# Kernel optimization log

Hardware: AMD Instinct MI355X
Metric: run time of the kernel (lower is better)

## Reference

```python
import jax, jax.numpy as jnp
import numpy as np

B, S, D, H = 2, 2048, 1024, 16
DH = D // H

def setup_inputs() -> dict:
    key = jax.random.key(0)
    ks = jax.random.split(key, 6)
    scale = 0.02
    return {
        "x":  jax.random.normal(ks[0], (B, S, D), jnp.float32),
        "Wq": jax.random.normal(ks[1], (D, D), jnp.float32) * scale,
        "Wk": jax.random.normal(ks[2], (D, D), jnp.float32) * scale,
        "Wv": jax.random.normal(ks[3], (D, D), jnp.float32) * scale,
        "Wo": jax.random.normal(ks[4], (D, D), jnp.float32) * scale,
        "bo": jnp.zeros((D,), jnp.float32),
    }

def reference(x, Wq, Wk, Wv, Wo, bo):
    b, s, d = x.shape
    h, dh = H, DH
    # projections -> [b, h, s, dh]
    def split_heads(t):
        return t.reshape(b, s, h, dh).transpose(0, 2, 1, 3)
    q = split_heads(x @ Wq)
    k = split_heads(x @ Wk)
    v = split_heads(x @ Wv)
    # scaled causal attention
    scores = jnp.einsum('bhqd,bhkd->bhqk', q, k) / jnp.sqrt(jnp.float32(dh))
    causal = jnp.tril(jnp.ones((s, s), bool))
    scores = jnp.where(causal[None, None], scores, -jnp.inf)
    attn = jax.nn.softmax(scores, axis=-1)
    # dropout p=0.0 -> identity
    ctx = jnp.einsum('bhqk,bhkd->bhqd', attn, v)
    ctx = ctx.transpose(0, 2, 1, 3).reshape(b, s, d)
    return ctx @ Wo + bo
```

## Files before the change

### kernel.cpp

```cpp
#include <hip/hip_runtime.h>


typedef _Float16 f16;
typedef _Float16 f16x8 __attribute__((ext_vector_type(8)));
typedef _Float16 f16x4 __attribute__((ext_vector_type(4)));
typedef float    f32x4 __attribute__((ext_vector_type(4)));

__device__ __forceinline__ void gload16(const void* g, void* l) {
  __builtin_amdgcn_global_load_lds(
      (const __attribute__((address_space(1))) void*)g,
      (__attribute__((address_space(3))) void*)l, 16, 0, 0);
}

__global__ void cvt_x(const float* __restrict__ x, f16* __restrict__ xb) {
  int idx = blockIdx.x * 256 + threadIdx.x;
  float4 v = ((const float4*)x)[idx];
  f16x4 o = { (f16)v.x, (f16)v.y, (f16)v.z, (f16)v.w };
  ((f16x4*)xb)[idx] = o;
}

__global__ void cvt_w(const float* __restrict__ W0, const float* __restrict__ W1,
                      const float* __restrict__ W2, const float* __restrict__ W3,
                      f16* __restrict__ T0, f16* __restrict__ T1,
                      f16* __restrict__ T2, f16* __restrict__ T3) {
  const float* W = blockIdx.z == 0 ? W0 : blockIdx.z == 1 ? W1 : blockIdx.z == 2 ? W2 : W3;
  f16*        Tt = blockIdx.z == 0 ? T0 : blockIdx.z == 1 ? T1 : blockIdx.z == 2 ? T2 : T3;
  __shared__ f16 tile[64][65];
  int tid = threadIdx.x;
  int k0 = blockIdx.y * 64, n0 = blockIdx.x * 64;
  int rr = tid >> 4, cc = (tid & 15) * 4;
#pragma unroll
  for (int p = 0; p < 4; ++p) {
    int r = rr + p * 16;
    float4 v = *(const float4*)(W + (size_t)(k0 + r) * 1024 + n0 + cc);
    tile[r][cc + 0] = (f16)v.x; tile[r][cc + 1] = (f16)v.y;
    tile[r][cc + 2] = (f16)v.z; tile[r][cc + 3] = (f16)v.w;
  }
  __syncthreads();
#pragma unroll
  for (int p = 0; p < 4; ++p) {
    int r = rr + p * 16;
    f16x4 v;
#pragma unroll
    for (int j = 0; j < 4; ++j) v[j] = tile[cc + j][r];
    *(f16x4*)(Tt + (size_t)(n0 + r) * 1024 + k0 + cc) = v;
  }
}

template <int MODE>
__global__ __launch_bounds__(256, 2)
void gemm_k(const f16* __restrict__ A, const f16* __restrict__ Bt,
            f16* __restrict__ oQ, f16* __restrict__ oK, f16* __restrict__ oV,
            float* __restrict__ oO, const float* __restrict__ bias) {
  constexpr int Kd = 1024;
  constexpr int BN = (MODE == 2) ? 64 : 128;
  constexpr int NF = BN / 32;
  __shared__ f16 smem[128 * 64 + BN * 64];
  f16* sA = smem;
  f16* sB = smem + 128 * 64;
  const int tid = threadIdx.x;
  const int lane = tid & 63, wid = tid >> 6;
  const int wr = wid >> 1, wc = wid & 1;
  const int bm = blockIdx.y * 128, bn = blockIdx.x * BN;

  f32x4 acc[4][NF] = {};

  for (int k0 = 0; k0 < Kd; k0 += 64) {
#pragma unroll
    for (int p = 0; p < 4; ++p) {
      int c = p * 256 + tid;
      int row = c >> 3;
      int gc = (c & 7) ^ (row & 7);
      gload16(A + (size_t)(bm + row) * Kd + k0 + gc * 8, sA + c * 8);
    }
#pragma unroll
    for (int p = 0; p < NF; ++p) {
      int c = p * 256 + tid;
      int row = c >> 3;
      int gc = (c & 7) ^ (row & 7);
      gload16(Bt + (size_t)(bn + row) * Kd + k0 + gc * 8, sB + c * 8);
    }
    __syncthreads();
#pragma unroll
    for (int ks = 0; ks < 2; ++ks) {
      f16x8 af[4], bf[NF];
#pragma unroll
      for (int m = 0; m < 4; ++m) {
        int row = wr * 64 + m * 16 + (lane & 15);
        int j = (ks * 4 + (lane >> 4)) ^ (row & 7);
        af[m] = *(const f16x8*)((const char*)sA + row * 128 + j * 16);
      }
#pragma unroll
      for (int n = 0; n < NF; ++n) {
        int row = wc * (BN / 2) + n * 16 + (lane & 15);
        int j = (ks * 4 + (lane >> 4)) ^ (row & 7);
        bf[n] = *(const f16x8*)((const char*)sB + row * 128 + j * 16);
      }
#pragma unroll
      for (int m = 0; m < 4; ++m)
#pragma unroll
        for (int n = 0; n < NF; ++n)
          acc[m][n] = __builtin_amdgcn_mfma_f32_16x16x32_f16(af[m], bf[n], acc[m][n], 0, 0, 0);
    }
    __syncthreads();
  }

  if constexpr (MODE == 2) {
#pragma unroll
    for (int m = 0; m < 4; ++m) {
      int rbase = bm + wr * 64 + m * 16 + ((lane >> 4) << 2);
#pragma unroll
      for (int n = 0; n < NF; ++n) {
        int ncol = bn + wc * (BN / 2) + n * 16 + (lane & 15);
        float bv = bias[ncol];
#pragma unroll
        for (int i = 0; i < 4; ++i)
          oO[(size_t)(rbase + i) * 1024 + ncol] = acc[m][n][i] + bv;
      }
    }
  } else {
    const int seg = bn >> 10;
    if (seg < 2) {
      f16* dst = seg == 0 ? oQ : oK;
#pragma unroll
      for (int m = 0; m < 4; ++m) {
        int rbase = bm + wr * 64 + m * 16 + ((lane >> 4) << 2);
#pragma unroll
        for (int n = 0; n < NF; ++n) {
          int ncol = (bn & 1023) + wc * 64 + n * 16 + (lane & 15);
          int h = ncol >> 6, dh = ncol & 63;
#pragma unroll
          for (int i = 0; i < 4; ++i) {
            int rr = rbase + i;
            int b = rr >> 11, s = rr & 2047;
            dst[(((size_t)(b * 16 + h) * 2048 + s) << 6) + dh] = (f16)acc[m][n][i];
          }
        }
      }
    } else {
      f16* T64 = smem;
      int b = bm >> 11, sbase = bm & 2047;
      int bnl = bn & 1023;
#pragma unroll
      for (int p = 0; p < 2; ++p) {
        if (wr == p) {
#pragma unroll
          for (int m = 0; m < 4; ++m)
#pragma unroll
            for (int n = 0; n < NF; ++n)
#pragma unroll
              for (int i = 0; i < 4; ++i) {
                int rl = m * 16 + ((lane >> 4) << 2) + i;
                int col = wc * 64 + n * 16 + (lane & 15);
                T64[rl * 132 + col] = (f16)acc[m][n][i];
              }
        }
        __syncthreads();
#pragma unroll
        for (int it = 0; it < 4; ++it) {
          int oc = it * 256 + tid;
          int ocol = oc >> 3;
          int och = oc & 7;
          f16x8 v;
#pragma unroll
          for (int j = 0; j < 8; ++j) v[j] = T64[(och * 8 + j) * 132 + ocol];
          int ncol = bnl + ocol;
          int h = ncol >> 6, dh = ncol & 63;
          *(f16x8*)(oV + ((size_t)((b * 16 + h) * 64 + dh) << 11) + sbase + p * 64 + och * 8) = v;
        }
        __syncthreads();
      }
    }
  }
}

__global__ __launch_bounds__(256, 2)
void attn_k(const f16* __restrict__ Q, const f16* __restrict__ Kg,
            const f16* __restrict__ Vt, f16* __restrict__ ctx) {
  __shared__ f16 sK[64 * 64];
  __shared__ f16 sV[64 * 64];
  __shared__ f16 sP[4][16 * 64];
  const int tid = threadIdx.x, lane = tid & 63, wid = tid >> 6;
  const int bh = blockIdx.y;
  const int b = bh >> 4, h = bh & 15;
  const int qt = ((bh >> 3) & 1) ? (31 - (int)blockIdx.x) : (int)blockIdx.x;
  const f16* Qb = Q + ((size_t)bh << 17);
  const f16* Kb = Kg + ((size_t)bh << 17);
  const f16* Vb = Vt + ((size_t)bh << 17);
  const float SC = 0.1803368801f;

  const int qbase = qt * 64 + wid * 16;
  const int qg = qbase + (lane & 15);
  const int qmax_w = qbase + 15;

  const int qrow_a = qbase + (lane & 15);
  f16x8 qf[2];
  qf[0] = *(const f16x8*)(Qb + (size_t)qrow_a * 64 + ((lane >> 4) << 3));
  qf[1] = *(const f16x8*)(Qb + (size_t)qrow_a * 64 + 32 + ((lane >> 4) << 3));

  f32x4 acc[4] = {};
  float m_run = -INFINITY, l_run = 0.f;

  for (int kt = 0; kt <= qt; ++kt) {
#pragma unroll
    for (int p = 0; p < 2; ++p) {
      int c = p * 256 + tid;
      int row = c >> 3;
      int gc = (c & 7) ^ (row & 7);
      gload16(Kb + (size_t)(kt * 64 + row) * 64 + gc * 8, sK + c * 8);
      gload16(Vb + (size_t)row * 2048 + kt * 64 + gc * 8, sV + c * 8);
    }
    __syncthreads();

    f32x4 sf[4];
#pragma unroll
    for (int kc = 0; kc < 4; ++kc) {
      if (kt * 64 + kc * 16 <= qmax_w) {
        f32x4 z = {};
#pragma unroll
        for (int ks = 0; ks < 2; ++ks) {
          int row = kc * 16 + (lane & 15);
          int j = (ks * 4 + (lane >> 4)) ^ (row & 7);
          f16x8 kf = *(const f16x8*)((const char*)sK + row * 128 + j * 16);
          z = __builtin_amdgcn_mfma_f32_16x16x32_f16(kf, qf[ks], z, 0, 0, 0);
        }
        sf[kc] = z;
      } else {
        sf[kc] = (f32x4){-1e30f, -1e30f, -1e30f, -1e30f};
      }
    }
#pragma unroll
    for (int kc = 0; kc < 4; ++kc) {
      if (kt * 64 + kc * 16 + 15 > qbase) {
#pragma unroll
        for (int i = 0; i < 4; ++i) {
          int kg = kt * 64 + kc * 16 + ((lane >> 4) << 2) + i;
          sf[kc][i] = (kg <= qg) ? sf[kc][i] * SC : -1e30f;
        }
      } else {
#pragma unroll
        for (int i = 0; i < 4; ++i) sf[kc][i] *= SC;
      }
    }
    float v01 = fmaxf(fmaxf(sf[0][0], sf[0][1]), fmaxf(sf[0][2], sf[0][3]));
    float v23 = fmaxf(fmaxf(sf[1][0], sf[1][1]), fmaxf(sf[1][2], sf[1][3]));
    float v45 = fmaxf(fmaxf(sf[2][0], sf[2][1]), fmaxf(sf[2][2], sf[2][3]));
    float v67 = fmaxf(fmaxf(sf[3][0], sf[3][1]), fmaxf(sf[3][2], sf[3][3]));
    float v = fmaxf(fmaxf(v01, v23), fmaxf(v45, v67));
    v = fmaxf(v, __shfl_xor(v, 16));
    v = fmaxf(v, __shfl_xor(v, 32));
    float mn = fmaxf(m_run, v);
    float scl = __builtin_amdgcn_exp2f(m_run - mn);
    m_run = mn;
    float ls = 0.f;
#pragma unroll
    for (int kc = 0; kc < 4; ++kc)
#pragma unroll
      for (int i = 0; i < 4; ++i) {
        float p = __builtin_amdgcn_exp2f(sf[kc][i] - mn);
        sf[kc][i] = p;
        ls += p;
      }
    ls += __shfl_xor(ls, 16);
    ls += __shfl_xor(ls, 32);
    l_run = l_run * scl + ls;
#pragma unroll
    for (int i = 0; i < 4; ++i) {
      float sb = __shfl(scl, ((lane >> 4) << 2) + i);
#pragma unroll
      for (int d = 0; d < 4; ++d) acc[d][i] *= sb;
    }
    char* Pw = (char*)(sP[wid]);
#pragma unroll
    for (int kc = 0; kc < 4; ++kc) {
      int kbase = kc * 16 + ((lane >> 4) << 2);
      int ch = kbase >> 3;
      f16x4 pv = { (f16)sf[kc][0], (f16)sf[kc][1], (f16)sf[kc][2], (f16)sf[kc][3] };
      *(f16x4*)(Pw + (lane & 15) * 128 + ((ch ^ (lane & 7)) << 4) + ((kbase & 7) << 1)) = pv;
    }
#pragma unroll
    for (int kk = 0; kk < 2; ++kk) {
      if (kt * 64 + kk * 32 <= qmax_w) {
        int prow = lane & 15;
        int pj = (kk * 4 + (lane >> 4)) ^ (prow & 7);
        f16x8 pa = *(const f16x8*)(Pw + prow * 128 + pj * 16);
#pragma unroll
        for (int d = 0; d < 4; ++d) {
          int vrow = d * 16 + (lane & 15);
          int vj = (kk * 4 + (lane >> 4)) ^ (vrow & 7);
          f16x8 vf = *(const f16x8*)((const char*)sV + vrow * 128 + vj * 16);
          acc[d] = __builtin_amdgcn_mfma_f32_16x16x32_f16(pa, vf, acc[d], 0, 0, 0);
        }
      }
    }
    __syncthreads();
  }
#pragma unroll
  for (int i = 0; i < 4; ++i) {
    float lb = __shfl(l_run, ((lane >> 4) << 2) + i);
    float r = 1.f / lb;
    int s = qbase + ((lane >> 4) << 2) + i;
#pragma unroll
    for (int d = 0; d < 4; ++d) {
      float val = acc[d][i] * r;
      ctx[((size_t)(b * 2048 + s) << 10) + (h << 6) + (d << 4) + (lane & 15)] = (f16)val;
    }
  }
}

extern "C" void kernel_launch(void* const* d_in, const int* in_sizes, int n_in,
                              void* d_out, int out_size, void* d_ws, size_t ws_size,
                              hipStream_t stream) {
  const float* x  = (const float*)d_in[0];
  const float* Wq = (const float*)d_in[1];
  const float* Wk = (const float*)d_in[2];
  const float* Wv = (const float*)d_in[3];
  const float* Wo = (const float*)d_in[4];
  const float* bo = (const float*)d_in[5];
  char* ws = (char*)d_ws;
  f16* xb   = (f16*)(ws);
  f16* Wcat = (f16*)(ws + ((size_t)8  << 20));
  f16* Wot  = (f16*)(ws + ((size_t)14 << 20));
  f16* Qb   = (f16*)(ws + ((size_t)16 << 20));
  f16* Kb   = (f16*)(ws + ((size_t)24 << 20));
  f16* Vtb  = (f16*)(ws + ((size_t)32 << 20));
  f16* ctx  = (f16*)(ws + ((size_t)40 << 20));
  const size_t MM = (size_t)1024 * 1024;

  hipLaunchKernelGGL(cvt_x, dim3(4096), dim3(256), 0, stream, x, xb);
  hipLaunchKernelGGL(cvt_w, dim3(16, 16, 4), dim3(256), 0, stream,
                     Wq, Wk, Wv, Wo, Wcat, Wcat + MM, Wcat + 2 * MM, Wot);
  hipLaunchKernelGGL((gemm_k<0>), dim3(24, 32), dim3(256), 0, stream,
                     xb, Wcat, Qb, Kb, Vtb, nullptr, nullptr);
  hipLaunchKernelGGL(attn_k, dim3(32, 32), dim3(256), 0, stream, Qb, Kb, Vtb, ctx);
  hipLaunchKernelGGL((gemm_k<2>), dim3(16, 32), dim3(256), 0, stream,
                     ctx, Wot, nullptr, nullptr, nullptr, (float*)d_out, bo);
}
```

Baseline: 188.2 us.

## Double attention query tile to 128 rows so each K/V load serves two row groups

Each attention block now handles 128 query rows instead of 64, with every wave owning two 16-row groups that keep separate softmax state and accumulators. Each K/V tile staged in shared memory is reused by twice as many queries, roughly halving the global-to-LDS K/V traffic and the barrier count per unit of work. The costs are half as many blocks (512), more registers per thread under a two-blocks-per-CU launch bound, and the two groups of a wave running one after the other within each K tile.

```diff
diff --git a/kernel.cpp b/kernel.cpp
--- a/kernel.cpp
+++ b/kernel.cpp
@@ -183,25 +183,28 @@
   const int tid = threadIdx.x, lane = tid & 63, wid = tid >> 6;
   const int bh = blockIdx.y;
   const int b = bh >> 4, h = bh & 15;
-  const int qt = ((bh >> 3) & 1) ? (31 - (int)blockIdx.x) : (int)blockIdx.x;
+  const int qt = ((bh >> 4) & 1) ? (15 - (int)blockIdx.x) : (int)blockIdx.x;
   const f16* Qb = Q + ((size_t)bh << 17);
   const f16* Kb = Kg + ((size_t)bh << 17);
   const f16* Vb = Vt + ((size_t)bh << 17);
   const float SC = 0.1803368801f;
 
-  const int qbase = qt * 64 + wid * 16;
-  const int qg = qbase + (lane & 15);
-  const int qmax_w = qbase + 15;
-
-  const int qrow_a = qbase + (lane & 15);
-  f16x8 qf[2];
-  qf[0] = *(const f16x8*)(Qb + (size_t)qrow_a * 64 + ((lane >> 4) << 3));
-  qf[1] = *(const f16x8*)(Qb + (size_t)qrow_a * 64 + 32 + ((lane >> 4) << 3));
-
-  f32x4 acc[4] = {};
-  float m_run = -INFINITY, l_run = 0.f;
-
-  for (int kt = 0; kt <= qt; ++kt) {
+  int qbase[2];
+  qbase[0] = qt * 128 + wid * 32;
+  qbase[1] = qbase[0] + 16;
+  f16x8 qf[2][2];
+#pragma unroll
+  for (int g = 0; g < 2; ++g) {
+    const f16* qp = Qb + (size_t)(qbase[g] + (lane & 15)) * 64 + ((lane >> 4) << 3);
+    qf[g][0] = *(const f16x8*)(qp);
+    qf[g][1] = *(const f16x8*)(qp + 32);
+  }
+
+  f32x4 acc[2][4] = {};
+  float m_run[2] = {-INFINITY, -INFINITY}, l_run[2] = {0.f, 0.f};
+  const int nkt = 2 * qt + 2;
+
+  for (int kt = 0; kt < nkt; ++kt) {
 #pragma unroll
     for (int p = 0; p < 2; ++p) {
       int c = p * 256 + tid;
@@ -212,100 +215,110 @@
     }
     __syncthreads();
 
-    f32x4 sf[4];
-#pragma unroll
-    for (int kc = 0; kc < 4; ++kc) {
-      if (kt * 64 + kc * 16 <= qmax_w) {
-        f32x4 z = {};
-#pragma unroll
-        for (int ks = 0; ks < 2; ++ks) {
-          int row = kc * 16 + (lane & 15);
-          int j = (ks * 4 + (lane >> 4)) ^ (row & 7);
-          f16x8 kf = *(const f16x8*)((const char*)sK + row * 128 + j * 16);
-          z = __builtin_amdgcn_mfma_f32_16x16x32_f16(kf, qf[ks], z, 0, 0, 0);
-        }
-        sf[kc] = z;
-      } else {
-        sf[kc] = (f32x4){-1e30f, -1e30f, -1e30f, -1e30f};
-      }
-    }
-#pragma unroll
-    for (int kc = 0; kc < 4; ++kc) {
-      if (kt * 64 + kc * 16 + 15 > qbase) {
+    char* Pw = (char*)(sP[wid]);
+#pragma unroll
+    for (int g = 0; g < 2; ++g) {
+      const int qb = qbase[g];
+      const int qg = qb + (lane & 15);
+      const int qmax_w = qb + 15;
+      if (kt * 64 > qmax_w) continue;
+
+      f32x4 sf[4];
+#pragma unroll
+      for (int kc = 0; kc < 4; ++kc) {
+        if (kt * 64 + kc * 16 <= qmax_w) {
+          f32x4 z = {};
+#pragma unroll
+          for (int ks = 0; ks < 2; ++ks) {
+            int row = kc * 16 + (lane & 15);
+            int j = (ks * 4 + (lane >> 4)) ^ (row & 7);
+            f16x8 kf = *(const f16x8*)((const char*)sK + row * 128 + j * 16);
+            z = __builtin_amdgcn_mfma_f32_16x16x32_f16(kf, qf[g][ks], z, 0, 0, 0);
+          }
+          sf[kc] = z;
+        } else {
+          sf[kc] = (f32x4){-1e30f, -1e30f, -1e30f, -1e30f};
+        }
+      }
+#pragma unroll
+      for (int kc = 0; kc < 4; ++kc) {
+        if (kt * 64 + kc * 16 + 15 > qb) {
+#pragma unroll
+          for (int i = 0; i < 4; ++i) {
+            int kg = kt * 64 + kc * 16 + ((lane >> 4) << 2) + i;
+            sf[kc][i] = (kg <= qg) ? sf[kc][i] * SC : -1e30f;
+          }
+        } else {
+#pragma unroll
+          for (int i = 0; i < 4; ++i) sf[kc][i] *= SC;
+        }
+      }
+      float v01 = fmaxf(fmaxf(sf[0][0], sf[0][1]), fmaxf(sf[0][2], sf[0][3]));
+      float v23 = fmaxf(fmaxf(sf[1][0], sf[1][1]), fmaxf(sf[1][2], sf[1][3]));
+      float v45 = fmaxf(fmaxf(sf[2][0], sf[2][1]), fmaxf(sf[2][2], sf[2][3]));
+      float v67 = fmaxf(fmaxf(sf[3][0], sf[3][1]), fmaxf(sf[3][2], sf[3][3]));
+      float v = fmaxf(fmaxf(v01, v23), fmaxf(v45, v67));
+      v = fmaxf(v, __shfl_xor(v, 16));
+      v = fmaxf(v, __shfl_xor(v, 32));
+      float mn = fmaxf(m_run[g], v);
+      float scl = __builtin_amdgcn_exp2f(m_run[g] - mn);
+      m_run[g] = mn;
+      float ls = 0.f;
+#pragma unroll
+      for (int kc = 0; kc < 4; ++kc)
 #pragma unroll
         for (int i = 0; i < 4; ++i) {
-          int kg = kt * 64 + kc * 16 + ((lane >> 4) << 2) + i;
-          sf[kc][i] = (kg <= qg) ? sf[kc][i] * SC : -1e30f;
-        }
-      } else {
-#pragma unroll
-        for (int i = 0; i < 4; ++i) sf[kc][i] *= SC;
-      }
-    }
-    float v01 = fmaxf(fmaxf(sf[0][0], sf[0][1]), fmaxf(sf[0][2], sf[0][3]));
-    float v23 = fmaxf(fmaxf(sf[1][0], sf[1][1]), fmaxf(sf[1][2], sf[1][3]));
-    float v45 = fmaxf(fmaxf(sf[2][0], sf[2][1]), fmaxf(sf[2][2], sf[2][3]));
-    float v67 = fmaxf(fmaxf(sf[3][0], sf[3][1]), fmaxf(sf[3][2], sf[3][3]));
-    float v = fmaxf(fmaxf(v01, v23), fmaxf(v45, v67));
-    v = fmaxf(v, __shfl_xor(v, 16));
-    v = fmaxf(v, __shfl_xor(v, 32));
-    float mn = fmaxf(m_run, v);
-    float scl = __builtin_amdgcn_exp2f(m_run - mn);
-    m_run = mn;
-    float ls = 0.f;
-#pragma unroll
-    for (int kc = 0; kc < 4; ++kc)
+          float p = __builtin_amdgcn_exp2f(sf[kc][i] - mn);
+          sf[kc][i] = p;
+          ls += p;
+        }
+      ls += __shfl_xor(ls, 16);
+      ls += __shfl_xor(ls, 32);
+      l_run[g] = l_run[g] * scl + ls;
 #pragma unroll
       for (int i = 0; i < 4; ++i) {
-        float p = __builtin_amdgcn_exp2f(sf[kc][i] - mn);
-        sf[kc][i] = p;
-        ls += p;
-      }
-    ls += __shfl_xor(ls, 16);
-    ls += __shfl_xor(ls, 32);
-    l_run = l_run * scl + ls;
+        float sb = __shfl(scl, ((lane >> 4) << 2) + i);
+#pragma unroll
+        for (int d = 0; d < 4; ++d) acc[g][d][i] *= sb;
+      }
+#pragma unroll
+      for (int kc = 0; kc < 4; ++kc) {
+        int kbase = kc * 16 + ((lane >> 4) << 2);
+        int ch = kbase >> 3;
+        f16x4 pv = { (f16)sf[kc][0], (f16)sf[kc][1], (f16)sf[kc][2], (f16)sf[kc][3] };
+        *(f16x4*)(Pw + (lane & 15) * 128 + ((ch ^ (lane & 7)) << 4) + ((kbase & 7) << 1)) = pv;
+      }
+#pragma unroll
+      for (int kk = 0; kk < 2; ++kk) {
+        if (kt * 64 + kk * 32 <= qmax_w) {
+          int prow = lane & 15;
+          int pj = (kk * 4 + (lane >> 4)) ^ (prow & 7);
+          f16x8 pa = *(const f16x8*)(Pw + prow * 128 + pj * 16);
+#pragma unroll
+          for (int d = 0; d < 4; ++d) {
+            int vrow = d * 16 + (lane & 15);
+            int vj = (kk * 4 + (lane >> 4)) ^ (vrow & 7);
+            f16x8 vf = *(const f16x8*)((const char*)sV + vrow * 128 + vj * 16);
+            acc[g][d] = __builtin_amdgcn_mfma_f32_16x16x32_f16(pa, vf, acc[g][d], 0, 0, 0);
+          }
+        }
+      }
+    }
+    __syncthreads();
+  }
+#pragma unroll
+  for (int g = 0; g < 2; ++g)
 #pragma unroll
     for (int i = 0; i < 4; ++i) {
-      float sb = __shfl(scl, ((lane >> 4) << 2) + i);
-#pragma unroll
-      for (int d = 0; d < 4; ++d) acc[d][i] *= sb;
-    }
-    char* Pw = (char*)(sP[wid]);
-#pragma unroll
-    for (int kc = 0; kc < 4; ++kc) {
-      int kbase = kc * 16 + ((lane >> 4) << 2);
-      int ch = kbase >> 3;
-      f16x4 pv = { (f16)sf[kc][0], (f16)sf[kc][1], (f16)sf[kc][2], (f16)sf[kc][3] };
-      *(f16x4*)(Pw + (lane & 15) * 128 + ((ch ^ (lane & 7)) << 4) + ((kbase & 7) << 1)) = pv;
-    }
-#pragma unroll
-    for (int kk = 0; kk < 2; ++kk) {
-      if (kt * 64 + kk * 32 <= qmax_w) {
-        int prow = lane & 15;
-        int pj = (kk * 4 + (lane >> 4)) ^ (prow & 7);
-        f16x8 pa = *(const f16x8*)(Pw + prow * 128 + pj * 16);
-#pragma unroll
-        for (int d = 0; d < 4; ++d) {
-          int vrow = d * 16 + (lane & 15);
-          int vj = (kk * 4 + (lane >> 4)) ^ (vrow & 7);
-          f16x8 vf = *(const f16x8*)((const char*)sV + vrow * 128 + vj * 16);
-          acc[d] = __builtin_amdgcn_mfma_f32_16x16x32_f16(pa, vf, acc[d], 0, 0, 0);
-        }
-      }
-    }
-    __syncthreads();
-  }
-#pragma unroll
-  for (int i = 0; i < 4; ++i) {
-    float lb = __shfl(l_run, ((lane >> 4) << 2) + i);
-    float r = 1.f / lb;
-    int s = qbase + ((lane >> 4) << 2) + i;
-#pragma unroll
-    for (int d = 0; d < 4; ++d) {
-      float val = acc[d][i] * r;
-      ctx[((size_t)(b * 2048 + s) << 10) + (h << 6) + (d << 4) + (lane & 15)] = (f16)val;
-    }
-  }
+      float lb = __shfl(l_run[g], ((lane >> 4) << 2) + i);
+      float r = 1.f / lb;
+      int s = qbase[g] + ((lane >> 4) << 2) + i;
+#pragma unroll
+      for (int d = 0; d < 4; ++d) {
+        float val = acc[g][d][i] * r;
+        ctx[((size_t)(b * 2048 + s) << 10) + (h << 6) + (d << 4) + (lane & 15)] = (f16)val;
+      }
+    }
 }
 
 extern "C" void kernel_launch(void* const* d_in, const int* in_sizes, int n_in,
@@ -332,7 +345,7 @@
                      Wq, Wk, Wv, Wo, Wcat, Wcat + MM, Wcat + 2 * MM, Wot);
   hipLaunchKernelGGL((gemm_k<0>), dim3(24, 32), dim3(256), 0, stream,
                      xb, Wcat, Qb, Kb, Vtb, nullptr, nullptr);
-  hipLaunchKernelGGL(attn_k, dim3(32, 32), dim3(256), 0, stream, Qb, Kb, Vtb, ctx);
+  hipLaunchKernelGGL(attn_k, dim3(16, 32), dim3(256), 0, stream, Qb, Kb, Vtb, ctx);
   hipLaunchKernelGGL((gemm_k<2>), dim3(16, 32), dim3(256), 0, stream,
                      ctx, Wot, nullptr, nullptr, nullptr, (float*)d_out, bo);
 }
```

Result: slower. 212.4 us (+12.9%).
